# Kernel optimization log

Hardware: AMD Instinct MI355X
Metric: run time of the kernel (lower is better)

The kernel has to match this reference:

```python
import jax, jax.numpy as jnp
import numpy as np

N, E, IN_DIM, H, D, EDGE_DIM, T = 50000, 800000, 128, 4, 32, 32, 8
NEG_SLOPE = 0.2


def setup_inputs() -> dict:
    key = jax.random.key(0)
    ks = jax.random.split(key, 12)
    s = 0.1  # xavier-ish scale
    return {
        "h": jax.random.normal(ks[0], (N, IN_DIM), jnp.float32),
        "W": jax.random.normal(ks[1], (IN_DIM, D * H), jnp.float32) * s,
        "edge_emb": jax.random.normal(ks[2], (T, EDGE_DIM), jnp.float32) * s,
        "W_r": jax.random.normal(ks[3], (T, EDGE_DIM, EDGE_DIM * H), jnp.float32) * s,
        "a_l": jax.random.normal(ks[4], (1, H, D), jnp.float32) * s,
        "a_r": jax.random.normal(ks[5], (1, H, D), jnp.float32) * s,
        "a_e": jax.random.normal(ks[6], (1, H, EDGE_DIM), jnp.float32) * s,
        "res_w": jax.random.normal(ks[7], (IN_DIM, D * H), jnp.float32) * s,
        "res_b": jnp.zeros((D * H,), jnp.float32),
        "row": jax.random.randint(ks[8], (E,), 0, N),  # src node per edge
        "col": jax.random.randint(ks[9], (E,), 0, N),  # dst node per edge
        "etype": jax.random.randint(ks[10], (E,), 0, T),
    }


def reference(h, W, edge_emb, W_r, a_l, a_r, a_e, res_w, res_b, row, col, etype):
    # node projection: [N, H, D]
    emb = (h @ W).reshape(-1, H, D)

    # TypedLinear on edge-type embeddings. Since edge features depend only on
    # etype, compute the per-type result once, then gather per edge.
    e_t = jnp.einsum('te,tef->tf', edge_emb, W_r).reshape(T, H, EDGE_DIM)
    h_e_t = (a_e * e_t).sum(-1)            # [T, H]

    h_l = (a_l * emb).sum(-1)              # [N, H]
    h_r = (a_r * emb).sum(-1)              # [N, H]
    scores = h_l[row] + h_r[col] + h_e_t[etype]          # [E, H]
    scores = jax.nn.leaky_relu(scores, NEG_SLOPE)

    # segment softmax over edges sharing the same destination node (col)
    m = jax.ops.segment_max(scores, col, num_segments=N)  # [N, H]
    ex = jnp.exp(scores - m[col])
    denom = jax.ops.segment_sum(ex, col, num_segments=N)
    alpha = ex / denom[col]                # [E, H]

    # u_mul_e + scatter-sum to destination nodes
    msg = emb[row] * alpha[:, :, None]     # [E, H, D]
    agg = jax.ops.segment_sum(msg, col, num_segments=N)   # [N, H, D]

    # original permutes to [N, D, H] before flattening (d-major layout)
    out = jnp.transpose(agg, (0, 2, 1)).reshape(-1, D * H)
    out = out + h @ res_w + res_b          # residual
    return jax.nn.elu(out)
```

## Files before the change

kernel.cpp:

```cpp
#include <hip/hip_runtime.h>
#include <math.h>

#define NH 4
#define EDIM 32
#define NEG_SLOPE 0.2f
#define BSH 5
#define BCAP 1024

typedef __attribute__((ext_vector_type(8))) short short8;
typedef __attribute__((ext_vector_type(4))) float f32x4;
typedef __attribute__((ext_vector_type(2))) float f32x2;

__device__ __forceinline__ unsigned short f2bf(float f) {
    unsigned int x = __builtin_bit_cast(unsigned int, f);
    unsigned int r = (x + 0x7fffu + ((x >> 16) & 1u)) >> 16;
    return (unsigned short)r;
}
__device__ __forceinline__ float bf2f(unsigned short u) {
    unsigned int x = ((unsigned int)u) << 16;
    return __builtin_bit_cast(float, x);
}

__global__ __launch_bounds__(256) void k_prep_fill(
    const float* __restrict__ W, const float* __restrict__ Rw,
    unsigned short* __restrict__ Wt, unsigned short* __restrict__ Rwt,
    const float* __restrict__ edge_emb, const float* __restrict__ W_r,
    const float* __restrict__ a_e, float* __restrict__ h_e_t,
    const int* __restrict__ row, const int* __restrict__ col,
    const int* __restrict__ etype, int* __restrict__ bucket_cursor,
    unsigned* __restrict__ ebuf, int E, int NB, int T)
{
    __shared__ int bins[2048];
    __shared__ int base[2048];
    int tid = threadIdx.x;
    int bid = blockIdx.x;

    if (bid < 64) {
        int idx = bid * 256 + tid;
        int n = idx >> 7, k = idx & 127;
        Wt[n * 128 + k]  = f2bf(W[k * 128 + n]);
        Rwt[n * 128 + k] = f2bf(Rw[k * 128 + n]);
        return;
    }
    if (bid < 64 + T * 4) {
        int j = bid - 64;
        int t = j >> 2;
        int ec = (j & 3) * 2 + (tid >> 7);
        int rem = tid & 127;
        float v = 0.f;
#pragma unroll
        for (int u = 0; u < 4; ++u) {
            int e = ec * 4 + u;
            v += edge_emb[t * EDIM + e] * W_r[(size_t)(t * EDIM + e) * 128 + rem];
        }
        v *= a_e[rem];
#pragma unroll
        for (int off = 16; off >= 1; off >>= 1)
            v += __shfl_xor(v, off);
        if ((rem & 31) == 0) atomicAdd(&h_e_t[t * NH + (rem >> 5)], v);
        return;
    }

    int fb = bid - 64 - T * 4;
    for (int i = tid; i < NB; i += 256) bins[i] = 0;
    __syncthreads();
    int lo = fb * 4096;
    int ccol[16];
#pragma unroll
    for (int u = 0; u < 16; ++u) {
        int i = lo + tid + u * 256;
        int c = (i < E) ? col[i] : -1;
        ccol[u] = c;
        if (c >= 0) atomicAdd(&bins[c >> BSH], 1);
    }
    __syncthreads();
    for (int i = tid; i < NB; i += 256) {
        int c = bins[i];
        base[i] = c ? atomicAdd(&bucket_cursor[i], c) : 0;
        bins[i] = 0;
    }
    __syncthreads();
#pragma unroll
    for (int u = 0; u < 16; ++u) {
        int i = lo + tid + u * 256;
        int c = ccol[u];
        if (c >= 0) {
            int bk = c >> BSH;
            int p = bk * BCAP + base[bk] + atomicAdd(&bins[bk], 1);
            ebuf[p] = (unsigned)row[i] | ((unsigned)etype[i] << 16)
                    | ((unsigned)(c & 31) << 24);
        }
    }
}

__global__ __launch_bounds__(256) void k_gemm(
    const float* __restrict__ A, const unsigned short* __restrict__ Wt,
    const unsigned short* __restrict__ Rwt, const float* __restrict__ Rb,
    const float* __restrict__ a_l, const float* __restrict__ a_r,
    unsigned short* __restrict__ EmbBf, unsigned short* __restrict__ ResBf,
    float* __restrict__ h_l, float* __restrict__ h_r, int M)
{
    __shared__ char lds[49152];
    int tid = threadIdx.x;
    int m0 = blockIdx.x * 64;

#pragma unroll
    for (int i = 0; i < 4; ++i) {
        int c = tid + 256 * i;
        int r = c >> 4, kc = c & 15;
        int grow = m0 + r;
        float4 v0 = make_float4(0.f, 0.f, 0.f, 0.f), v1 = v0;
        if (grow < M) {
            v0 = *(const float4*)&A[(size_t)grow * 128 + kc * 8];
            v1 = *(const float4*)&A[(size_t)grow * 128 + kc * 8 + 4];
        }
        union { unsigned short u[8]; uint4 v; } p;
        p.u[0] = f2bf(v0.x); p.u[1] = f2bf(v0.y); p.u[2] = f2bf(v0.z); p.u[3] = f2bf(v0.w);
        p.u[4] = f2bf(v1.x); p.u[5] = f2bf(v1.y); p.u[6] = f2bf(v1.z); p.u[7] = f2bf(v1.w);
        int b = (r * 256 + kc * 16) ^ ((r & 7) << 4);
        *(uint4*)&lds[b] = p.v;
    }
#pragma unroll
    for (int i = 0; i < 8; ++i) {
        int c = tid + 256 * i;
        int n = c >> 4, kc = c & 15;
        uint4 v = *(const uint4*)&Wt[n * 128 + kc * 8];
        int b = 16384 + ((n * 256 + kc * 16) ^ ((n & 7) << 4));
        *(uint4*)&lds[b] = v;
    }
    __syncthreads();

    int w = tid >> 6, lane = tid & 63;
    int g = lane >> 4, l15 = lane & 15;
    int lrow = w * 16 + l15;

    short8 a[4];
#pragma unroll
    for (int s = 0; s < 4; ++s)
        a[s] = *(const short8*)&lds[(lrow * 256 + s * 64 + g * 16) ^ ((lrow & 7) << 4)];

    f32x4 acc[8];
#pragma unroll
    for (int f = 0; f < 8; ++f) acc[f] = (f32x4){0.f, 0.f, 0.f, 0.f};

#pragma unroll
    for (int f = 0; f < 8; ++f) {
        int n = f * 16 + l15;
        int nsw = (n & 7) << 4;
#pragma unroll
        for (int s = 0; s < 4; ++s) {
            short8 b = *(const short8*)&lds[16384 + ((n * 256 + s * 64 + g * 16) ^ nsw)];
            acc[f] = __builtin_amdgcn_mfma_f32_16x16x32_bf16(a[s], b, acc[f], 0, 0, 0);
        }
    }
#pragma unroll
    for (int f = 0; f < 8; ++f) {
        int col2 = f * 16 + l15;
#pragma unroll
        for (int reg = 0; reg < 4; ++reg) {
            int grow = m0 + w * 16 + g * 4 + reg;
            if (grow < M) EmbBf[(size_t)grow * 128 + col2] = f2bf(acc[f][reg]);
        }
    }
    {
        float alv[8], arv[8];
#pragma unroll
        for (int f = 0; f < 8; ++f) {
            alv[f] = a_l[f * 16 + l15];
            arv[f] = a_r[f * 16 + l15];
        }
#pragma unroll
        for (int reg = 0; reg < 4; ++reg) {
            float4 hl4, hr4;
#pragma unroll
            for (int hh = 0; hh < 4; ++hh) {
                float pl = alv[2 * hh] * acc[2 * hh][reg] + alv[2 * hh + 1] * acc[2 * hh + 1][reg];
                float pr = arv[2 * hh] * acc[2 * hh][reg] + arv[2 * hh + 1] * acc[2 * hh + 1][reg];
#pragma unroll
                for (int off = 8; off >= 1; off >>= 1) {
                    pl += __shfl_xor(pl, off);
                    pr += __shfl_xor(pr, off);
                }
                (&hl4.x)[hh] = pl;
                (&hr4.x)[hh] = pr;
            }
            int grow = m0 + w * 16 + g * 4 + reg;
            if (l15 == 0 && grow < M) {
                *(float4*)&h_l[(size_t)grow * 4] = hl4;
                *(float4*)&h_r[(size_t)grow * 4] = hr4;
            }
        }
    }

    __syncthreads();
#pragma unroll
    for (int i = 0; i < 8; ++i) {
        int c = tid + 256 * i;
        int n = c >> 4, kc = c & 15;
        uint4 v = *(const uint4*)&Rwt[n * 128 + kc * 8];
        int b = 16384 + ((n * 256 + kc * 16) ^ ((n & 7) << 4));
        *(uint4*)&lds[b] = v;
    }
    __syncthreads();

#pragma unroll
    for (int f = 0; f < 8; ++f) acc[f] = (f32x4){0.f, 0.f, 0.f, 0.f};
#pragma unroll
    for (int f = 0; f < 8; ++f) {
        int n = f * 16 + l15;
        int nsw = (n & 7) << 4;
#pragma unroll
        for (int s = 0; s < 4; ++s) {
            short8 b = *(const short8*)&lds[16384 + ((n * 256 + s * 64 + g * 16) ^ nsw)];
            acc[f] = __builtin_amdgcn_mfma_f32_16x16x32_bf16(a[s], b, acc[f], 0, 0, 0);
        }
    }
#pragma unroll
    for (int f = 0; f < 8; ++f) {
        int col2 = f * 16 + l15;
        float bias = Rb[col2];
#pragma unroll
        for (int reg = 0; reg < 4; ++reg) {
            int grow = m0 + w * 16 + g * 4 + reg;
            if (grow < M) ResBf[(size_t)grow * 128 + col2] = f2bf(acc[f][reg] + bias);
        }
    }
}

__global__ __launch_bounds__(256) void k_sort_aggregate(
    const unsigned* __restrict__ ebuf, const int* __restrict__ bucket_cursor,
    const float* __restrict__ h_l, const float* __restrict__ h_e_t,
    const float* __restrict__ h_r, const unsigned short* __restrict__ embBf,
    const unsigned short* __restrict__ resBf, float* __restrict__ out, int N)
{
    __shared__ int sedge[BCAP];
    __shared__ int cnt[32];
    __shared__ int scn[33];
    __shared__ char shalpha[4 * 1536];

    int b = blockIdx.x;
    int tid = threadIdx.x;
    int seg = b * BCAP;
    int m = bucket_cursor[b];

    if (tid < 32) cnt[tid] = 0;
    __syncthreads();
    for (int i = tid; i < m; i += 256)
        atomicAdd(&cnt[(ebuf[seg + i] >> 24) & 31], 1);
    __syncthreads();
    if (tid < 32) {
        int v = cnt[tid];
        int s = v;
#pragma unroll
        for (int off = 1; off < 32; off <<= 1) {
            int u2 = __shfl_up(s, off);
            if (tid >= off) s += u2;
        }
        scn[tid + 1] = s;
        if (tid == 0) scn[0] = 0;
        cnt[tid] = s - v;
    }
    __syncthreads();
    for (int i = tid; i < m; i += 256) {
        unsigned e = ebuf[seg + i];
        int p = atomicAdd(&cnt[(e >> 24) & 31], 1);
        sedge[p] = (int)(e & 0x00FFFFFFu);
    }
    __syncthreads();

    int w = tid >> 6, lane = tid & 63;
    int myh = lane >> 4;
    int l31 = lane & 31;
    int sel = lane >> 5;
    int hq = l31 >> 3;
    int loff = l31 * 8;
    char* wb = &shalpha[w * 1536];
    const char* ab2 = wb + 256 + hq * 260;
    const char* embByte = (const char*)embBf;

    for (int it = 0; it < 8; ++it) {
        int nd = it * 4 + w;
        int n = b * 32 + nd;
        if (n >= N) break;
        int st0 = scn[nd];
        int deg = scn[nd + 1] - st0;
        float4 hrv = *(const float4*)&h_r[(size_t)n * 4];

        if (deg <= 64) {
            bool act = lane < deg;
            float p0 = 0.f, p1 = 0.f, p2 = 0.f, p3 = 0.f;
            int roval = 0;
            if (act) {
                int pk = sedge[st0 + lane];
                roval = (pk & 0xffff) << 8;
                float4 hl = *(const float4*)&h_l[(size_t)(pk & 0xffff) * 4];
                float4 he = *(const float4*)&h_e_t[(size_t)(pk >> 16) * 4];
                float sc0 = hl.x + he.x + hrv.x; sc0 = sc0 > 0.f ? sc0 : NEG_SLOPE * sc0;
                float sc1 = hl.y + he.y + hrv.y; sc1 = sc1 > 0.f ? sc1 : NEG_SLOPE * sc1;
                float sc2 = hl.z + he.z + hrv.z; sc2 = sc2 > 0.f ? sc2 : NEG_SLOPE * sc2;
                float sc3 = hl.w + he.w + hrv.w; sc3 = sc3 > 0.f ? sc3 : NEG_SLOPE * sc3;
                p0 = __expf(sc0); p1 = __expf(sc1);
                p2 = __expf(sc2); p3 = __expf(sc3);
            }
            *(int*)(wb + lane * 4) = roval;
            *(float*)(wb + 256 + 0 * 260 + lane * 4) = p0;
            *(float*)(wb + 256 + 1 * 260 + lane * 4) = p1;
            *(float*)(wb + 256 + 2 * 260 + lane * 4) = p2;
            *(float*)(wb + 256 + 3 * 260 + lane * 4) = p3;

            float d0 = p0, d1 = p1, d2 = p2, d3 = p3;
#pragma unroll
            for (int off = 32; off >= 1; off >>= 1) {
                d0 += __shfl_xor(d0, off); d1 += __shfl_xor(d1, off);
                d2 += __shfl_xor(d2, off); d3 += __shfl_xor(d3, off);
            }
            float den = hq == 0 ? d0 : hq == 1 ? d1 : hq == 2 ? d2 : d3;
            float inv = (deg > 0) ? __builtin_amdgcn_rcpf(den) : 0.f;

            f32x4 acc4 = (f32x4){0.f, 0.f, 0.f, 0.f};
            for (int q = 0; q < deg; q += 8) {
                int ro[4]; float aq[4];
#pragma unroll
                for (int u = 0; u < 4; ++u) {
                    int qe = q + 2 * u + sel;
                    ro[u] = *(const int*)(wb + qe * 4);
                    aq[u] = *(const float*)(ab2 + qe * 4);
                }
                uint2 ev[4];
#pragma unroll
                for (int u = 0; u < 4; ++u)
                    ev[u] = *(const uint2*)(embByte + (size_t)(unsigned)(ro[u] + loff));
#pragma unroll
                for (int u = 0; u < 4; ++u) {
                    f32x4 ef;
                    ef.x = __builtin_bit_cast(float, ev[u].x << 16);
                    ef.y = __builtin_bit_cast(float, ev[u].x & 0xffff0000u);
                    ef.z = __builtin_bit_cast(float, ev[u].y << 16);
                    ef.w = __builtin_bit_cast(float, ev[u].y & 0xffff0000u);
                    acc4 = __builtin_elementwise_fma(
                        ef, (f32x4){aq[u], aq[u], aq[u], aq[u]}, acc4);
                }
            }
            acc4.x += __shfl_xor(acc4.x, 32);
            acc4.y += __shfl_xor(acc4.y, 32);
            acc4.z += __shfl_xor(acc4.z, 32);
            acc4.w += __shfl_xor(acc4.w, 32);
            float vlo = sel ? acc4.z : acc4.x;
            float vhi = sel ? acc4.w : acc4.y;

            int j0 = l31 * 4 + sel * 2;
            int h0 = j0 >> 5, dd = j0 & 31;
            size_t ob = (size_t)n * 128;
            float o0 = vlo * inv + bf2f(resBf[ob + dd * 4 + h0]);
            float o1 = vhi * inv + bf2f(resBf[ob + (dd + 1) * 4 + h0]);
            out[ob + dd * 4 + h0] = o0 > 0.f ? o0 : expm1f(o0);
            out[ob + (dd + 1) * 4 + h0] = o1 > 0.f ? o1 : expm1f(o1);
        } else {
            f32x2 acc2 = (f32x2){0.f, 0.f};
            float d0 = 0.f, d1 = 0.f, d2 = 0.f, d3 = 0.f;
            for (int base2 = 0; base2 < deg; base2 += 64) {
                int el = base2 + lane;
                if (el < deg) {
                    int pk = sedge[st0 + el];
                    float4 hl = *(const float4*)&h_l[(size_t)(pk & 0xffff) * 4];
                    float4 he = *(const float4*)&h_e_t[(size_t)(pk >> 16) * 4];
                    float sc0 = hl.x + he.x + hrv.x; sc0 = sc0 > 0.f ? sc0 : NEG_SLOPE * sc0;
                    float sc1 = hl.y + he.y + hrv.y; sc1 = sc1 > 0.f ? sc1 : NEG_SLOPE * sc1;
                    float sc2 = hl.z + he.z + hrv.z; sc2 = sc2 > 0.f ? sc2 : NEG_SLOPE * sc2;
                    float sc3 = hl.w + he.w + hrv.w; sc3 = sc3 > 0.f ? sc3 : NEG_SLOPE * sc3;
                    d0 += __expf(sc0); d1 += __expf(sc1);
                    d2 += __expf(sc2); d3 += __expf(sc3);
                }
            }
#pragma unroll
            for (int off = 32; off >= 1; off >>= 1) {
                d0 += __shfl_xor(d0, off); d1 += __shfl_xor(d1, off);
                d2 += __shfl_xor(d2, off); d3 += __shfl_xor(d3, off);
            }
            float den = myh == 0 ? d0 : myh == 1 ? d1 : myh == 2 ? d2 : d3;
            float inv = __builtin_amdgcn_rcpf(den);
            for (int base2 = 0; base2 < deg; base2 += 64) {
                int el = base2 + lane;
                float p0 = 0.f, p1 = 0.f, p2 = 0.f, p3 = 0.f;
                int r = 0;
                if (el < deg) {
                    int pk = sedge[st0 + el];
                    r = pk & 0xffff;
                    float4 hl = *(const float4*)&h_l[(size_t)r * 4];
                    float4 he = *(const float4*)&h_e_t[(size_t)(pk >> 16) * 4];
                    float sc0 = hl.x + he.x + hrv.x; sc0 = sc0 > 0.f ? sc0 : NEG_SLOPE * sc0;
                    float sc1 = hl.y + he.y + hrv.y; sc1 = sc1 > 0.f ? sc1 : NEG_SLOPE * sc1;
                    float sc2 = hl.z + he.z + hrv.z; sc2 = sc2 > 0.f ? sc2 : NEG_SLOPE * sc2;
                    float sc3 = hl.w + he.w + hrv.w; sc3 = sc3 > 0.f ? sc3 : NEG_SLOPE * sc3;
                    p0 = __expf(sc0); p1 = __expf(sc1);
                    p2 = __expf(sc2); p3 = __expf(sc3);
                }
                int cmax = (deg - base2 < 64) ? (deg - base2) : 64;
                for (int qq = 0; qq < cmax; ++qq) {
                    int rq = __shfl(r, qq);
                    float a0 = __shfl(p0, qq), a1 = __shfl(p1, qq);
                    float a2 = __shfl(p2, qq), a3 = __shfl(p3, qq);
                    float aqv = myh == 0 ? a0 : myh == 1 ? a1 : myh == 2 ? a2 : a3;
                    unsigned int ev = *(const unsigned int*)&embBf[(size_t)rq * 128 + lane * 2];
                    f32x2 ef;
                    ef.x = __builtin_bit_cast(float, ev << 16);
                    ef.y = __builtin_bit_cast(float, ev & 0xffff0000u);
                    acc2 = __builtin_elementwise_fma(ef, (f32x2){aqv, aqv}, acc2);
                }
            }
            int j0 = lane * 2;
            int h0 = j0 >> 5, dd0 = j0 & 31;
            size_t ob = (size_t)n * 128;
            float o0 = acc2.x * inv + bf2f(resBf[ob + dd0 * 4 + h0]);
            float o1 = acc2.y * inv + bf2f(resBf[ob + (dd0 + 1) * 4 + h0]);
            out[ob + dd0 * 4 + h0] = o0 > 0.f ? o0 : expm1f(o0);
            out[ob + (dd0 + 1) * 4 + h0] = o1 > 0.f ? o1 : expm1f(o1);
        }
    }
}

extern "C" void kernel_launch(void* const* d_in, const int* in_sizes, int n_in,
                              void* d_out, int out_size, void* d_ws, size_t ws_size,
                              hipStream_t stream)
{
    const float* h        = (const float*)d_in[0];
    const float* W        = (const float*)d_in[1];
    const float* edge_emb = (const float*)d_in[2];
    const float* W_r      = (const float*)d_in[3];
    const float* a_l      = (const float*)d_in[4];
    const float* a_r      = (const float*)d_in[5];
    const float* a_e      = (const float*)d_in[6];
    const float* res_w    = (const float*)d_in[7];
    const float* res_b    = (const float*)d_in[8];
    const int*   row      = (const int*)d_in[9];
    const int*   col      = (const int*)d_in[10];
    const int*   etype    = (const int*)d_in[11];
    float* out = (float*)d_out;

    int N = in_sizes[0] / 128;
    int E = in_sizes[9];
    int T = in_sizes[2] / EDIM;
    int NB = (N + 31) >> BSH;

    char* ws = (char*)d_ws;
    size_t off = 0;
    auto alloc = [&](size_t bytes) -> char* {
        char* p = ws + off;
        off = (off + bytes + 255) & ~(size_t)255;
        return p;
    };
    unsigned short* embBf = (unsigned short*)alloc((size_t)N * 128 * 2);
    unsigned short* resBf = (unsigned short*)alloc((size_t)N * 128 * 2);
    unsigned short* Wt    = (unsigned short*)alloc((size_t)128 * 128 * 2);
    unsigned short* Rwt   = (unsigned short*)alloc((size_t)128 * 128 * 2);
    float* h_l   = (float*)alloc((size_t)N * 4 * 4);
    float* h_r   = (float*)alloc((size_t)N * 4 * 4);
    int* bucket_cursor = (int*)alloc(2048 * 4);
    float* h_e_t = (float*)alloc((size_t)T * NH * 4);
    unsigned* ebuf = (unsigned*)alloc((size_t)(NB + 1) * BCAP * 4);

    int nFill = (E + 4095) / 4096;
    int nGemm = (N + 63) / 64;

    hipMemsetAsync(bucket_cursor, 0, 8192 + (size_t)T * NH * 4, stream);
    hipLaunchKernelGGL(k_prep_fill, dim3(64 + T * 4 + nFill), dim3(256), 0, stream,
                       W, res_w, Wt, Rwt, edge_emb, W_r, a_e, h_e_t,
                       row, col, etype, bucket_cursor, ebuf, E, NB, T);
    hipLaunchKernelGGL(k_gemm, dim3(nGemm), dim3(256), 0, stream,
                       h, Wt, Rwt, res_b, a_l, a_r, embBf, resBf, h_l, h_r, N);
    hipLaunchKernelGGL(k_sort_aggregate, dim3(NB), dim3(256), 0, stream,
                       ebuf, bucket_cursor, h_l, h_e_t, h_r, embBf, resBf, out, N);
}
```

Measured before the change: 99.00 us.

## Merge edge bucketing into GEMM kernel, drop memset, halve GEMM LDS

The memset is removed: bucket_cursor is now zeroed in the prep kernel, and h_e_t is computed per type without atomics. The edge bucket-fill blocks move from the prep kernel into the GEMM kernel, so fill and GEMM blocks run concurrently in one launch. The GEMM now stages B in two 64-column halves to cut LDS from 48KB to 32KB, which should raise occupancy. The cost is extra syncthreads in the GEMM blocks and a mix of heterogeneous block types in one grid.

```diff
diff --git a/kernel.cpp b/kernel.cpp
--- a/kernel.cpp
+++ b/kernel.cpp
@@ -21,89 +21,86 @@
     return __builtin_bit_cast(float, x);
 }
 
-__global__ __launch_bounds__(256) void k_prep_fill(
+__global__ __launch_bounds__(256) void k_prep(
     const float* __restrict__ W, const float* __restrict__ Rw,
     unsigned short* __restrict__ Wt, unsigned short* __restrict__ Rwt,
+    int* __restrict__ bucket_cursor,
     const float* __restrict__ edge_emb, const float* __restrict__ W_r,
-    const float* __restrict__ a_e, float* __restrict__ h_e_t,
-    const int* __restrict__ row, const int* __restrict__ col,
-    const int* __restrict__ etype, int* __restrict__ bucket_cursor,
-    unsigned* __restrict__ ebuf, int E, int NB, int T)
+    const float* __restrict__ a_e, float* __restrict__ h_e_t)
 {
-    __shared__ int bins[2048];
-    __shared__ int base[2048];
     int tid = threadIdx.x;
-    int bid = blockIdx.x;
-
-    if (bid < 64) {
-        int idx = bid * 256 + tid;
+    if (blockIdx.x < 64) {
+        int idx = blockIdx.x * 256 + tid;
         int n = idx >> 7, k = idx & 127;
         Wt[n * 128 + k]  = f2bf(W[k * 128 + n]);
         Rwt[n * 128 + k] = f2bf(Rw[k * 128 + n]);
+        if (idx < 2048) bucket_cursor[idx] = 0;
         return;
     }
-    if (bid < 64 + T * 4) {
-        int j = bid - 64;
-        int t = j >> 2;
-        int ec = (j & 3) * 2 + (tid >> 7);
-        int rem = tid & 127;
+    int t = blockIdx.x - 64;
+    if (tid < 128) {
+        int rem = tid;
         float v = 0.f;
 #pragma unroll
-        for (int u = 0; u < 4; ++u) {
-            int e = ec * 4 + u;
+        for (int e = 0; e < EDIM; ++e)
             v += edge_emb[t * EDIM + e] * W_r[(size_t)(t * EDIM + e) * 128 + rem];
-        }
         v *= a_e[rem];
 #pragma unroll
         for (int off = 16; off >= 1; off >>= 1)
             v += __shfl_xor(v, off);
-        if ((rem & 31) == 0) atomicAdd(&h_e_t[t * NH + (rem >> 5)], v);
-        return;
-    }
-
-    int fb = bid - 64 - T * 4;
-    for (int i = tid; i < NB; i += 256) bins[i] = 0;
-    __syncthreads();
-    int lo = fb * 4096;
-    int ccol[16];
-#pragma unroll
-    for (int u = 0; u < 16; ++u) {
-        int i = lo + tid + u * 256;
-        int c = (i < E) ? col[i] : -1;
-        ccol[u] = c;
-        if (c >= 0) atomicAdd(&bins[c >> BSH], 1);
-    }
-    __syncthreads();
-    for (int i = tid; i < NB; i += 256) {
-        int c = bins[i];
-        base[i] = c ? atomicAdd(&bucket_cursor[i], c) : 0;
-        bins[i] = 0;
-    }
-    __syncthreads();
-#pragma unroll
-    for (int u = 0; u < 16; ++u) {
-        int i = lo + tid + u * 256;
-        int c = ccol[u];
-        if (c >= 0) {
-            int bk = c >> BSH;
-            int p = bk * BCAP + base[bk] + atomicAdd(&bins[bk], 1);
-            ebuf[p] = (unsigned)row[i] | ((unsigned)etype[i] << 16)
-                    | ((unsigned)(c & 31) << 24);
-        }
-    }
-}
-
-__global__ __launch_bounds__(256) void k_gemm(
+        if ((rem & 31) == 0) h_e_t[t * NH + (rem >> 5)] = v;
+    }
+}
+
+__global__ __launch_bounds__(256) void k_gemm_fill(
     const float* __restrict__ A, const unsigned short* __restrict__ Wt,
     const unsigned short* __restrict__ Rwt, const float* __restrict__ Rb,
     const float* __restrict__ a_l, const float* __restrict__ a_r,
     unsigned short* __restrict__ EmbBf, unsigned short* __restrict__ ResBf,
-    float* __restrict__ h_l, float* __restrict__ h_r, int M)
+    float* __restrict__ h_l, float* __restrict__ h_r, int M,
+    const int* __restrict__ row, const int* __restrict__ col,
+    const int* __restrict__ etype, int* __restrict__ bucket_cursor,
+    unsigned* __restrict__ ebuf, int E, int NB, int nFill)
 {
-    __shared__ char lds[49152];
+    __shared__ char lds[32768];
     int tid = threadIdx.x;
-    int m0 = blockIdx.x * 64;
-
+
+    if ((int)blockIdx.x < nFill) {
+        int* bins = (int*)lds;
+        int* base = bins + 2048;
+        for (int i = tid; i < NB; i += 256) bins[i] = 0;
+        __syncthreads();
+        int lo = blockIdx.x * 4096;
+        int ccol[16];
+#pragma unroll
+        for (int u = 0; u < 16; ++u) {
+            int i = lo + tid + u * 256;
+            int c = (i < E) ? col[i] : -1;
+            ccol[u] = c;
+            if (c >= 0) atomicAdd(&bins[c >> BSH], 1);
+        }
+        __syncthreads();
+        for (int i = tid; i < NB; i += 256) {
+            int c = bins[i];
+            base[i] = c ? atomicAdd(&bucket_cursor[i], c) : 0;
+            bins[i] = 0;
+        }
+        __syncthreads();
+#pragma unroll
+        for (int u = 0; u < 16; ++u) {
+            int i = lo + tid + u * 256;
+            int c = ccol[u];
+            if (c >= 0) {
+                int bk = c >> BSH;
+                int p = bk * BCAP + base[bk] + atomicAdd(&bins[bk], 1);
+                ebuf[p] = (unsigned)row[i] | ((unsigned)etype[i] << 16)
+                        | ((unsigned)(c & 31) << 24);
+            }
+        }
+        return;
+    }
+
+    int m0 = ((int)blockIdx.x - nFill) * 64;
 #pragma unroll
     for (int i = 0; i < 4; ++i) {
         int c = tid + 256 * i;
@@ -120,20 +117,37 @@
         int b = (r * 256 + kc * 16) ^ ((r & 7) << 4);
         *(uint4*)&lds[b] = p.v;
     }
-#pragma unroll
-    for (int i = 0; i < 8; ++i) {
-        int c = tid + 256 * i;
-        int n = c >> 4, kc = c & 15;
-        uint4 v = *(const uint4*)&Wt[n * 128 + kc * 8];
-        int b = 16384 + ((n * 256 + kc * 16) ^ ((n & 7) << 4));
-        *(uint4*)&lds[b] = v;
-    }
-    __syncthreads();
 
     int w = tid >> 6, lane = tid & 63;
     int g = lane >> 4, l15 = lane & 15;
     int lrow = w * 16 + l15;
 
+    auto stageB = [&](const unsigned short* src) {
+#pragma unroll
+        for (int i = 0; i < 4; ++i) {
+            int c = tid + 256 * i;
+            int n2 = c >> 4, kc = c & 15;
+            uint4 v = *(const uint4*)&src[n2 * 128 + kc * 8];
+            int b = 16384 + ((n2 * 256 + kc * 16) ^ ((n2 & 7) << 4));
+            *(uint4*)&lds[b] = v;
+        }
+    };
+    auto computeHalf = [&](f32x4* accp, const short8* a) {
+#pragma unroll
+        for (int f = 0; f < 4; ++f) {
+            int n2 = f * 16 + l15;
+            int nsw = (n2 & 7) << 4;
+#pragma unroll
+            for (int s = 0; s < 4; ++s) {
+                short8 b = *(const short8*)&lds[16384 + ((n2 * 256 + s * 64 + g * 16) ^ nsw)];
+                accp[f] = __builtin_amdgcn_mfma_f32_16x16x32_bf16(a[s], b, accp[f], 0, 0, 0);
+            }
+        }
+    };
+
+    stageB(Wt);
+    __syncthreads();
+
     short8 a[4];
 #pragma unroll
     for (int s = 0; s < 4; ++s)
@@ -143,16 +157,12 @@
 #pragma unroll
     for (int f = 0; f < 8; ++f) acc[f] = (f32x4){0.f, 0.f, 0.f, 0.f};
 
-#pragma unroll
-    for (int f = 0; f < 8; ++f) {
-        int n = f * 16 + l15;
-        int nsw = (n & 7) << 4;
-#pragma unroll
-        for (int s = 0; s < 4; ++s) {
-            short8 b = *(const short8*)&lds[16384 + ((n * 256 + s * 64 + g * 16) ^ nsw)];
-            acc[f] = __builtin_amdgcn_mfma_f32_16x16x32_bf16(a[s], b, acc[f], 0, 0, 0);
-        }
-    }
+    computeHalf(&acc[0], a);
+    __syncthreads();
+    stageB(Wt + 64 * 128);
+    __syncthreads();
+    computeHalf(&acc[4], a);
+
 #pragma unroll
     for (int f = 0; f < 8; ++f) {
         int col2 = f * 16 + l15;
@@ -193,28 +203,16 @@
     }
 
     __syncthreads();
-#pragma unroll
-    for (int i = 0; i < 8; ++i) {
-        int c = tid + 256 * i;
-        int n = c >> 4, kc = c & 15;
-        uint4 v = *(const uint4*)&Rwt[n * 128 + kc * 8];
-        int b = 16384 + ((n * 256 + kc * 16) ^ ((n & 7) << 4));
-        *(uint4*)&lds[b] = v;
-    }
-    __syncthreads();
-
+    stageB(Rwt);
+    __syncthreads();
 #pragma unroll
     for (int f = 0; f < 8; ++f) acc[f] = (f32x4){0.f, 0.f, 0.f, 0.f};
-#pragma unroll
-    for (int f = 0; f < 8; ++f) {
-        int n = f * 16 + l15;
-        int nsw = (n & 7) << 4;
-#pragma unroll
-        for (int s = 0; s < 4; ++s) {
-            short8 b = *(const short8*)&lds[16384 + ((n * 256 + s * 64 + g * 16) ^ nsw)];
-            acc[f] = __builtin_amdgcn_mfma_f32_16x16x32_bf16(a[s], b, acc[f], 0, 0, 0);
-        }
-    }
+    computeHalf(&acc[0], a);
+    __syncthreads();
+    stageB(Rwt + 64 * 128);
+    __syncthreads();
+    computeHalf(&acc[4], a);
+
 #pragma unroll
     for (int f = 0; f < 8; ++f) {
         int col2 = f * 16 + l15;
@@ -455,19 +453,19 @@
     unsigned short* Rwt   = (unsigned short*)alloc((size_t)128 * 128 * 2);
     float* h_l   = (float*)alloc((size_t)N * 4 * 4);
     float* h_r   = (float*)alloc((size_t)N * 4 * 4);
+    float* h_e_t = (float*)alloc((size_t)T * NH * 4);
     int* bucket_cursor = (int*)alloc(2048 * 4);
-    float* h_e_t = (float*)alloc((size_t)T * NH * 4);
     unsigned* ebuf = (unsigned*)alloc((size_t)(NB + 1) * BCAP * 4);
 
     int nFill = (E + 4095) / 4096;
     int nGemm = (N + 63) / 64;
 
-    hipMemsetAsync(bucket_cursor, 0, 8192 + (size_t)T * NH * 4, stream);
-    hipLaunchKernelGGL(k_prep_fill, dim3(64 + T * 4 + nFill), dim3(256), 0, stream,
-                       W, res_w, Wt, Rwt, edge_emb, W_r, a_e, h_e_t,
-                       row, col, etype, bucket_cursor, ebuf, E, NB, T);
-    hipLaunchKernelGGL(k_gemm, dim3(nGemm), dim3(256), 0, stream,
-                       h, Wt, Rwt, res_b, a_l, a_r, embBf, resBf, h_l, h_r, N);
+    hipLaunchKernelGGL(k_prep, dim3(64 + T), dim3(256), 0, stream,
+                       W, res_w, Wt, Rwt, bucket_cursor,
+                       edge_emb, W_r, a_e, h_e_t);
+    hipLaunchKernelGGL(k_gemm_fill, dim3(nFill + nGemm), dim3(256), 0, stream,
+                       h, Wt, Rwt, res_b, a_l, a_r, embBf, resBf, h_l, h_r, N,
+                       row, col, etype, bucket_cursor, ebuf, E, NB, nFill);
     hipLaunchKernelGGL(k_sort_aggregate, dim3(NB), dim3(256), 0, stream,
                        ebuf, bucket_cursor, h_l, h_e_t, h_r, embBf, resBf, out, N);
 }
```

Result: faster. 86.49 us (-12.6%).
